# Optimization experiments

Measured on AMD Instinct MI355X. Metric: run time of the kernel, lower is better.

Reference implementation:

```python
import jax, jax.numpy as jnp
import numpy as np

EMBED = 512
MLP_DIM = 2048
B, T = 4, 4096
EPS = 1e-5


def setup_inputs() -> dict:
    key = jax.random.key(0)
    ks = jax.random.split(key, 8)
    s = lambda fan_in: 1.0 / np.sqrt(fan_in)
    inp = {
        "x": jax.random.normal(ks[0], (B, T, EMBED), dtype=jnp.float32),
        "Wq": jax.random.uniform(ks[1], (EMBED, EMBED), jnp.float32, -s(EMBED), s(EMBED)),
        "bq": jnp.zeros((EMBED,), jnp.float32),
        "Wk": jax.random.uniform(ks[2], (EMBED, EMBED), jnp.float32, -s(EMBED), s(EMBED)),
        "bk": jnp.zeros((EMBED,), jnp.float32),
        "Wv": jax.random.uniform(ks[3], (EMBED, EMBED), jnp.float32, -s(EMBED), s(EMBED)),
        "bv": jnp.zeros((EMBED,), jnp.float32),
        "W1": jax.random.uniform(ks[4], (EMBED, MLP_DIM), jnp.float32, -s(EMBED), s(EMBED)),
        "b1": jnp.zeros((MLP_DIM,), jnp.float32),
        "W2": jax.random.uniform(ks[5], (MLP_DIM, EMBED), jnp.float32, -s(MLP_DIM), s(MLP_DIM)),
        "b2": jnp.zeros((EMBED,), jnp.float32),
        "ln1_g": jnp.ones((EMBED,), jnp.float32),
        "ln1_b": jnp.zeros((EMBED,), jnp.float32),
        "ln2_g": jnp.ones((EMBED,), jnp.float32),
        "ln2_b": jnp.zeros((EMBED,), jnp.float32),
    }
    return inp


def _layernorm(x, g, b):
    mu = x.mean(-1, keepdims=True)
    var = ((x - mu) ** 2).mean(-1, keepdims=True)
    return (x - mu) * jax.lax.rsqrt(var + EPS) * g + b


def reference(x, Wq, bq, Wk, bk, Wv, bv, W1, b1, W2, b2, ln1_g, ln1_b, ln2_g, ln2_b):
    # pre-LN causal self-attention (single head)
    h = _layernorm(x, ln1_g, ln1_b)
    q = h @ Wq + bq  # [B,T,D]
    k = h @ Wk + bk
    v = h @ Wv + bv
    scale = 1.0 / jnp.sqrt(jnp.float32(EMBED))
    scores = jnp.einsum("btd,bsd->bts", q, k) * scale  # [B,T,T]
    mask = jnp.tril(jnp.ones((T, T), dtype=bool))
    scores = jnp.where(mask, scores, -jnp.inf)
    # NOTE: source applies softmax over the ENTIRE [T,T] matrix per batch
    # element (global max + global sum), not per-row. Replicate exactly.
    m = scores.max(axis=(-2, -1), keepdims=True)
    e = jnp.exp(scores - m)
    attn = e / e.sum(axis=(-2, -1), keepdims=True)
    x = x + jnp.einsum("bts,bsd->btd", attn, v)
    # MLP
    h2 = _layernorm(x, ln2_g, ln2_b)
    x = x + (jax.nn.gelu(h2 @ W1 + b1, approximate=False) @ W2 + b2)
    return x
```

## Files before the change

kernel.cpp:

```cpp
#include <hip/hip_runtime.h>
#include <hip/hip_bf16.h>
#include <math.h>

#define EMBED 512
#define MLPD  2048
#define NB    4
#define TS    4096
#define BT    (NB*TS)
#define BK    64
#define NTILES_TRI 528

typedef __attribute__((ext_vector_type(4))) float f32x4;
typedef __attribute__((ext_vector_type(8))) short s16x8;
typedef __hip_bfloat16 bf16_t;

__device__ __forceinline__ void gload16(const void* g, void* l) {
  __builtin_amdgcn_global_load_lds(
      (const __attribute__((address_space(1))) void*)g,
      (__attribute__((address_space(3))) void*)l, 16, 0, 0);
}

__device__ __forceinline__ float fast_erf(float y) {
  const float ay = fabsf(y);
  const float t = __builtin_amdgcn_rcpf(1.0f + 0.3275911f*ay);
  float poly = 1.061405429f;
  poly = poly*t - 1.453152027f;
  poly = poly*t + 1.421413741f;
  poly = poly*t - 0.284496736f;
  poly = poly*t + 0.254829592f;
  poly = poly*t;
  const float e = 1.0f - poly*__expf(-ay*ay);
  return copysignf(e, y);
}


__device__ __forceinline__ void gemm_core(
    const bf16_t* __restrict__ A, int lda,
    const bf16_t* __restrict__ Bt, int ldb,
    int kmax, bf16_t* Alds, bf16_t* Blds, f32x4 acc[4][4])
{
  const int tid = threadIdx.x;
  const int w  = tid >> 6;
  const int l  = tid & 63;
  const int wr = w >> 1, wc = w & 1;
  const int fr = l & 15, fg = l >> 4;

  #pragma unroll
  for (int i = 0; i < 4; ++i)
    #pragma unroll
    for (int j = 0; j < 4; ++j)
      #pragma unroll
      for (int e = 0; e < 4; ++e)
        acc[i][j][e] = 0.0f;

  const int srow = w*32 + (l >> 3);
  const int sx = (((l & 7) ^ ((l >> 3) & 7)))*8;
  const int rsw = fr & 7;

  for (int k0 = 0; k0 < kmax; k0 += BK) {
    __syncthreads();
    #pragma unroll
    for (int c = 0; c < 4; ++c) {
      const bf16_t* ga = A  + (size_t)(srow + c*8)*lda + (k0 + sx);
      const bf16_t* gb = Bt + (size_t)(srow + c*8)*ldb + (k0 + sx);
      gload16(ga, Alds + (w*32 + c*8)*BK);
      gload16(gb, Blds + (w*32 + c*8)*BK);
    }
    __syncthreads();
    #pragma unroll
    for (int kk = 0; kk < BK; kk += 32) {
      s16x8 av[4], bv[4];
      const int ch = (kk >> 3) + fg;
      const int co = (ch ^ rsw) << 3;
      #pragma unroll
      for (int mf = 0; mf < 4; ++mf)
        av[mf] = *(const s16x8*)(Alds + (wr*64 + mf*16 + fr)*BK + co);
      #pragma unroll
      for (int nf = 0; nf < 4; ++nf)
        bv[nf] = *(const s16x8*)(Blds + (wc*64 + nf*16 + fr)*BK + co);
      #pragma unroll
      for (int mf = 0; mf < 4; ++mf)
        #pragma unroll
        for (int nf = 0; nf < 4; ++nf)
          acc[mf][nf] = __builtin_amdgcn_mfma_f32_16x16x32_bf16(
              av[mf], bv[nf], acc[mf][nf], 0, 0, 0);
    }
  }
}

__device__ __forceinline__ void gemm_core_deep(
    const bf16_t* __restrict__ A, int lda,
    const bf16_t* __restrict__ Bt, int ldb,
    int kmax, bf16_t* Alds, bf16_t* Blds, f32x4 acc[4][4])
{
  const int tid = threadIdx.x;
  const int w  = tid >> 6;
  const int l  = tid & 63;
  const int wr = w >> 1, wc = w & 1;
  const int fr = l & 15, fg = l >> 4;

  #pragma unroll
  for (int i = 0; i < 4; ++i)
    #pragma unroll
    for (int j = 0; j < 4; ++j)
      #pragma unroll
      for (int e = 0; e < 4; ++e)
        acc[i][j][e] = 0.0f;

  const int srow = w*32 + (l >> 3);
  const int sx = (((l & 7) ^ ((l >> 3) & 7)))*8;
  const int rsw = fr & 7;
  const int T = kmax >> 6;

  #define ISSUE_A(t_) do { \
    bf16_t* dst = Alds + ((t_) % 3)*(128*BK); \
    const int k0_ = (t_)*BK; \
    _Pragma("unroll") \
    for (int c = 0; c < 4; ++c) \
      gload16(A + (size_t)(srow + c*8)*lda + (k0_ + sx), dst + (w*32 + c*8)*BK); \
  } while (0)
  #define ISSUE_B(t_) do { \
    bf16_t* dst = Blds + ((t_) & 1)*(128*BK); \
    const int k0_ = (t_)*BK; \
    _Pragma("unroll") \
    for (int c = 0; c < 4; ++c) \
      gload16(Bt + (size_t)(srow + c*8)*ldb + (k0_ + sx), dst + (w*32 + c*8)*BK); \
  } while (0)

  ISSUE_A(0); ISSUE_B(0);
  if (T > 1) ISSUE_A(1);

  for (int t = 0; t < T; ++t) {
    if (t <= T - 3) {
      ISSUE_B(t + 1); ISSUE_A(t + 2);
      asm volatile("s_waitcnt vmcnt(12)" ::: "memory");
    } else if (t == T - 2) {
      ISSUE_B(t + 1);
      asm volatile("s_waitcnt vmcnt(8)" ::: "memory");
    } else {
      asm volatile("s_waitcnt vmcnt(0)" ::: "memory");
    }
    __builtin_amdgcn_s_barrier();
    bf16_t* Ac = Alds + (t % 3)*(128*BK);
    bf16_t* Bc = Blds + (t & 1)*(128*BK);
    #pragma unroll
    for (int kk = 0; kk < BK; kk += 32) {
      s16x8 av[4], bv[4];
      const int ch = (kk >> 3) + fg;
      const int co = (ch ^ rsw) << 3;
      #pragma unroll
      for (int mf = 0; mf < 4; ++mf)
        av[mf] = *(const s16x8*)(Ac + (wr*64 + mf*16 + fr)*BK + co);
      #pragma unroll
      for (int nf = 0; nf < 4; ++nf)
        bv[nf] = *(const s16x8*)(Bc + (wc*64 + nf*16 + fr)*BK + co);
      #pragma unroll
      for (int mf = 0; mf < 4; ++mf)
        #pragma unroll
        for (int nf = 0; nf < 4; ++nf)
          acc[mf][nf] = __builtin_amdgcn_mfma_f32_16x16x32_bf16(
              av[mf], bv[nf], acc[mf][nf], 0, 0, 0);
    }
    __builtin_amdgcn_s_barrier();
  }
  #undef ISSUE_A
  #undef ISSUE_B
}

#define EPILOGUE_SETUP \
  const int l = threadIdx.x & 63; const int w = threadIdx.x >> 6; \
  const int wr = w >> 1, wc = w & 1, fr = l & 15, fg = l >> 4;

__global__ void __launch_bounds__(256) k_proj_qkv(
    const bf16_t* __restrict__ A,
    const bf16_t* __restrict__ wqt, const bf16_t* __restrict__ wkt,
    const bf16_t* __restrict__ wvt,
    const float* __restrict__ bq, const float* __restrict__ bk,
    const float* __restrict__ bv,
    bf16_t* __restrict__ qb, bf16_t* __restrict__ kb, bf16_t* __restrict__ vt)
{
  __shared__ __align__(16) bf16_t Alds[128*BK];
  __shared__ __align__(16) bf16_t Blds[128*BK];
  f32x4 acc[4][4];
  const int z = blockIdx.z;
  const bf16_t* Wt = (z == 0) ? wqt : (z == 1) ? wkt : wvt;
  const float* bias = (z == 0) ? bq : (z == 1) ? bk : bv;
  const int m0 = blockIdx.x*128, n0 = blockIdx.y*128;
  gemm_core(A + (size_t)m0*EMBED, EMBED, Wt + (size_t)n0*EMBED, EMBED, EMBED,
            Alds, Blds, acc);
  EPILOGUE_SETUP
  if (z < 2) {
    bf16_t* outp = (z == 0) ? qb : kb;
    #pragma unroll
    for (int mf = 0; mf < 4; ++mf)
      #pragma unroll
      for (int nf = 0; nf < 4; ++nf) {
        const int col = n0 + wc*64 + nf*16 + fr;
        const float bb = bias[col];
        #pragma unroll
        for (int j = 0; j < 4; ++j) {
          const int row = m0 + wr*64 + mf*16 + fg*4 + j;
          outp[(size_t)row*EMBED + col] = __float2bfloat16(acc[mf][nf][j] + bb);
        }
      }
  } else {
    #pragma unroll
    for (int mf = 0; mf < 4; ++mf)
      #pragma unroll
      for (int nf = 0; nf < 4; ++nf) {
        const int col = n0 + wc*64 + nf*16 + fr;
        const float bb = bias[col];
        #pragma unroll
        for (int j = 0; j < 4; ++j) {
          const int row = m0 + wr*64 + mf*16 + fg*4 + j;
          const int b = row >> 12, t = row & 4095;
          vt[((size_t)b*EMBED + col)*TS + t] = __float2bfloat16(acc[mf][nf][j] + bb);
        }
      }
  }
}

__global__ void __launch_bounds__(256) k_attn1(
    const bf16_t* __restrict__ q, const bf16_t* __restrict__ kmat,
    bf16_t* __restrict__ P, float* __restrict__ partials, int serial_b)
{
  __shared__ __align__(16) bf16_t Alds[128*BK];
  __shared__ __align__(16) bf16_t Blds[128*BK];
  int b, r;
  if (serial_b >= 0) {
    b = serial_b; r = blockIdx.x;
  } else {
    const int L = blockIdx.x;
    const int logical = (L & 7)*264 + (L >> 3);
    b = logical / NTILES_TRI;
    r = logical - b*NTILES_TRI;
  }
  int ti = (int)((sqrtf(8.0f*(float)r + 1.0f) - 1.0f)*0.5f);
  while ((ti + 1)*(ti + 2)/2 <= r) ++ti;
  while (ti*(ti + 1)/2 > r) --ti;
  const int tj = r - ti*(ti + 1)/2;

  f32x4 acc[4][4];
  const bf16_t* A  = q    + ((size_t)b*TS + (size_t)ti*128)*EMBED;
  const bf16_t* Bt = kmat + ((size_t)b*TS + (size_t)tj*128)*EMBED;
  gemm_core(A, EMBED, Bt, EMBED, EMBED, Alds, Blds, acc);

  EPILOGUE_SETUP
  bf16_t* Pb = P + (size_t)((serial_b >= 0) ? 0 : b)*TS*TS;
  const float SC = 0.044194173824159216f;
  float lsum = 0.0f;
  #pragma unroll
  for (int mf = 0; mf < 4; ++mf)
    #pragma unroll
    for (int nf = 0; nf < 4; ++nf) {
      const int gs = tj*128 + wc*64 + nf*16 + fr;
      #pragma unroll
      for (int j = 0; j < 4; ++j) {
        const int gt = ti*128 + wr*64 + mf*16 + fg*4 + j;
        float e = 0.0f;
        if (gs <= gt) e = __expf(acc[mf][nf][j]*SC - 30.0f);
        Pb[(size_t)gt*TS + gs] = __float2bfloat16(e);
        lsum += e;
      }
    }
  #pragma unroll
  for (int off = 32; off > 0; off >>= 1) lsum += __shfl_xor(lsum, off);
  __shared__ float red[4];
  if (l == 0) red[w] = lsum;
  __syncthreads();
  if (threadIdx.x == 0)
    partials[(size_t)b*NTILES_TRI + r] = red[0] + red[1] + red[2] + red[3];
}

__global__ void k_reduce(const float* __restrict__ part, float* __restrict__ S, int n)
{
  const int b = blockIdx.x;
  const int l = threadIdx.x;
  float s = 0.0f;
  for (int i = l; i < n; i += 64) s += part[(size_t)b*n + i];
  #pragma unroll
  for (int off = 32; off > 0; off >>= 1) s += __shfl_xor(s, off);
  if (l == 0) S[b] = s;
}

__global__ void __launch_bounds__(256) k_attn2(
    const bf16_t* __restrict__ P, const bf16_t* __restrict__ vt,
    const float* __restrict__ S, const float* __restrict__ x,
    float* __restrict__ out, int serial_b)
{
  __shared__ __align__(16) bf16_t Alds[3*128*BK];
  __shared__ __align__(16) bf16_t Blds[2*128*BK];
  int ti, nj, b;
  if (serial_b >= 0) {
    ti = blockIdx.x; nj = blockIdx.y; b = serial_b;
  } else {
    const int L = blockIdx.x;
    const int xc = L & 7;
    const int idx = L >> 3;
    nj = idx & 3;
    const int s = idx >> 2;
    b = s & 3;
    const int which = s >> 2;
    ti = (which == 0) ? 2*xc
       : (which == 1) ? 2*xc + 1
       : (which == 2) ? 30 - 2*xc
                      : 31 - 2*xc;
  }
  f32x4 acc[4][4];
  const bf16_t* A  = P + (size_t)((serial_b >= 0) ? 0 : b)*TS*TS + (size_t)ti*128*TS;
  const bf16_t* Bt = vt + ((size_t)b*EMBED + (size_t)nj*128)*TS;
  const int kmax = (ti + 1)*128;
  gemm_core_deep(A, TS, Bt, TS, kmax, Alds, Blds, acc);

  EPILOGUE_SETUP
  const float invS = 1.0f / S[b];
  #pragma unroll
  for (int mf = 0; mf < 4; ++mf)
    #pragma unroll
    for (int nf = 0; nf < 4; ++nf) {
      const int d = nj*128 + wc*64 + nf*16 + fr;
      #pragma unroll
      for (int j = 0; j < 4; ++j) {
        const int t = ti*128 + wr*64 + mf*16 + fg*4 + j;
        const size_t idx2 = ((size_t)b*TS + t)*EMBED + d;
        out[idx2] = x[idx2] + acc[mf][nf][j]*invS;
      }
    }
}

__global__ void __launch_bounds__(256) k_mlp1(
    const bf16_t* __restrict__ A, const bf16_t* __restrict__ Wt,
    const float* __restrict__ bias, bf16_t* __restrict__ mid)
{
  __shared__ __align__(16) bf16_t Alds[128*BK];
  __shared__ __align__(16) bf16_t Blds[128*BK];
  f32x4 acc[4][4];
  const int m0 = blockIdx.x*128, n0 = blockIdx.y*128;
  gemm_core(A + (size_t)m0*EMBED, EMBED, Wt + (size_t)n0*EMBED, EMBED, EMBED,
            Alds, Blds, acc);
  EPILOGUE_SETUP
  #pragma unroll
  for (int mf = 0; mf < 4; ++mf)
    #pragma unroll
    for (int nf = 0; nf < 4; ++nf) {
      const int col = n0 + wc*64 + nf*16 + fr;
      const float bb = bias[col];
      #pragma unroll
      for (int j = 0; j < 4; ++j) {
        const int row = m0 + wr*64 + mf*16 + fg*4 + j;
        const float pre = acc[mf][nf][j] + bb;
        const float ge = 0.5f*pre*(1.0f + fast_erf(pre*0.70710678118654752f));
        mid[(size_t)row*MLPD + col] = __float2bfloat16(ge);
      }
    }
}

__global__ void __launch_bounds__(256) k_mlp2(
    const bf16_t* __restrict__ A, const bf16_t* __restrict__ Wt,
    const float* __restrict__ bias, float* __restrict__ out)
{
  __shared__ __align__(16) bf16_t Alds[3*128*BK];
  __shared__ __align__(16) bf16_t Blds[2*128*BK];
  f32x4 acc[4][4];
  const int m0 = blockIdx.x*128, n0 = blockIdx.y*128;
  gemm_core_deep(A + (size_t)m0*MLPD, MLPD, Wt + (size_t)n0*MLPD, MLPD, MLPD,
                 Alds, Blds, acc);
  EPILOGUE_SETUP
  #pragma unroll
  for (int mf = 0; mf < 4; ++mf)
    #pragma unroll
    for (int nf = 0; nf < 4; ++nf) {
      const int col = n0 + wc*64 + nf*16 + fr;
      const float bb = bias[col];
      #pragma unroll
      for (int j = 0; j < 4; ++j) {
        const int row = m0 + wr*64 + mf*16 + fg*4 + j;
        const size_t idx = (size_t)row*EMBED + col;
        out[idx] = out[idx] + acc[mf][nf][j] + bb;
      }
    }
}

__global__ void __launch_bounds__(256) k_ln(
    const float* __restrict__ x, const float* __restrict__ g,
    const float* __restrict__ bta, bf16_t* __restrict__ h)
{
  const int row = blockIdx.x*4 + (threadIdx.x >> 6);
  const int l = threadIdx.x & 63;
  const float4* xr = (const float4*)(x + (size_t)row*EMBED);
  const float4 a = xr[l*2], c = xr[l*2 + 1];
  float vals[8] = {a.x, a.y, a.z, a.w, c.x, c.y, c.z, c.w};
  float s = 0.0f, ss = 0.0f;
  #pragma unroll
  for (int i = 0; i < 8; ++i) { s += vals[i]; ss += vals[i]*vals[i]; }
  #pragma unroll
  for (int off = 32; off > 0; off >>= 1) {
    s  += __shfl_xor(s,  off);
    ss += __shfl_xor(ss, off);
  }
  const float mu = s*(1.0f/EMBED);
  const float var = ss*(1.0f/EMBED) - mu*mu;
  const float rs = rsqrtf(var + 1e-5f);
  const float4* g4 = (const float4*)g;
  const float4* b4 = (const float4*)bta;
  const float4 ga = g4[l*2], gc = g4[l*2 + 1];
  const float4 ba = b4[l*2], bc = b4[l*2 + 1];
  const float gv[8] = {ga.x, ga.y, ga.z, ga.w, gc.x, gc.y, gc.z, gc.w};
  const float bv[8] = {ba.x, ba.y, ba.z, ba.w, bc.x, bc.y, bc.z, bc.w};
  s16x8 ov;
  bf16_t* ovp = (bf16_t*)&ov;
  #pragma unroll
  for (int i = 0; i < 8; ++i)
    ovp[i] = __float2bfloat16((vals[i] - mu)*rs*gv[i] + bv[i]);
  *((s16x8*)(h + (size_t)row*EMBED) + l) = ov;
}

__global__ void __launch_bounds__(256) k_transpose_all(
    const float* __restrict__ Wq, const float* __restrict__ Wk,
    const float* __restrict__ Wv, const float* __restrict__ W1,
    const float* __restrict__ W2,
    bf16_t* __restrict__ wqt, bf16_t* __restrict__ wkt,
    bf16_t* __restrict__ wvt, bf16_t* __restrict__ w1t,
    bf16_t* __restrict__ w2t)
{
  __shared__ float tile[32][33];
  int L = blockIdx.x;
  const float* W; bf16_t* Wt; int Kd, Nd, t;
  if (L < 768) {
    const int m = L >> 8; t = L & 255;
    W  = (m == 0) ? Wq : (m == 1) ? Wk : Wv;
    Wt = (m == 0) ? wqt : (m == 1) ? wkt : wvt;
    Kd = EMBED; Nd = EMBED;
  } else if (L < 1792) {
    t = L - 768;  W = W1; Wt = w1t; Kd = EMBED; Nd = MLPD;
  } else {
    t = L - 1792; W = W2; Wt = w2t; Kd = MLPD; Nd = EMBED;
  }
  const int ntx = Nd >> 5;
  const int tx32 = (t % ntx)*32, ty32 = (t / ntx)*32;
  const int x = threadIdx.x & 31, y8 = threadIdx.x >> 5;
  #pragma unroll
  for (int r = 0; r < 4; ++r) {
    const int y = y8 + r*8;
    tile[y][x] = W[(size_t)(ty32 + y)*Nd + tx32 + x];
  }
  __syncthreads();
  #pragma unroll
  for (int r = 0; r < 4; ++r) {
    const int y = y8 + r*8;
    Wt[(size_t)(tx32 + y)*Kd + ty32 + x] = __float2bfloat16(tile[x][y]);
  }
}

extern "C" void kernel_launch(void* const* d_in, const int* in_sizes, int n_in,
                              void* d_out, int out_size, void* d_ws, size_t ws_size,
                              hipStream_t stream) {
  (void)in_sizes; (void)n_in; (void)out_size;
  const float* x   = (const float*)d_in[0];
  const float* Wq  = (const float*)d_in[1];
  const float* bq  = (const float*)d_in[2];
  const float* Wk  = (const float*)d_in[3];
  const float* bk  = (const float*)d_in[4];
  const float* Wv  = (const float*)d_in[5];
  const float* bv  = (const float*)d_in[6];
  const float* W1  = (const float*)d_in[7];
  const float* b1  = (const float*)d_in[8];
  const float* W2  = (const float*)d_in[9];
  const float* b2  = (const float*)d_in[10];
  const float* g1  = (const float*)d_in[11];
  const float* be1 = (const float*)d_in[12];
  const float* g2  = (const float*)d_in[13];
  const float* be2 = (const float*)d_in[14];
  float* out = (float*)d_out;

  char* p = (char*)d_ws;
  auto alloc = [&](size_t bytes) -> char* {
    char* r = p; p += (bytes + 255) & ~(size_t)255; return r;
  };
  bf16_t* h   = (bf16_t*)alloc((size_t)BT*EMBED*2);
  bf16_t* wqt = (bf16_t*)alloc((size_t)EMBED*EMBED*2);
  bf16_t* wkt = (bf16_t*)alloc((size_t)EMBED*EMBED*2);
  bf16_t* wvt = (bf16_t*)alloc((size_t)EMBED*EMBED*2);
  bf16_t* w1t = (bf16_t*)alloc((size_t)MLPD*EMBED*2);
  bf16_t* w2t = (bf16_t*)alloc((size_t)EMBED*MLPD*2);
  bf16_t* qb  = (bf16_t*)alloc((size_t)BT*EMBED*2);
  bf16_t* kb  = (bf16_t*)alloc((size_t)BT*EMBED*2);
  bf16_t* vtb = (bf16_t*)alloc((size_t)BT*EMBED*2);
  float* partials = (float*)alloc((size_t)NB*NTILES_TRI*sizeof(float));
  float* S = (float*)alloc(256);

  const size_t mid_bytes = (size_t)BT*MLPD*2;
  const size_t p_full    = (size_t)NB*TS*TS*2;
  const size_t used = (size_t)(p - (char*)d_ws);
  const bool full = ws_size >= used + (p_full > mid_bytes ? p_full : mid_bytes);
  char* region = alloc(full ? p_full : mid_bytes);
  bf16_t* P   = (bf16_t*)region;
  bf16_t* mid = (bf16_t*)region;

  k_transpose_all<<<dim3(2816), 256, 0, stream>>>(Wq, Wk, Wv, W1, W2,
                                                  wqt, wkt, wvt, w1t, w2t);
  k_ln<<<BT/4, 256, 0, stream>>>(x, g1, be1, h);

  k_proj_qkv<<<dim3(BT/128, EMBED/128, 3), 256, 0, stream>>>(
      h, wqt, wkt, wvt, bq, bk, bv, qb, kb, vtb);

  if (full) {
    k_attn1<<<dim3(NB*NTILES_TRI), 256, 0, stream>>>(qb, kb, P, partials, -1);
    k_reduce<<<NB, 64, 0, stream>>>(partials, S, NTILES_TRI);
    k_attn2<<<dim3(512), 256, 0, stream>>>(P, vtb, S, x, out, -1);
  } else {
    for (int b = 0; b < NB; ++b) {
      k_attn1<<<dim3(NTILES_TRI), 256, 0, stream>>>(qb, kb, P, partials, b);
      k_reduce<<<1, 64, 0, stream>>>(partials + (size_t)b*NTILES_TRI, S + b, NTILES_TRI);
      k_attn2<<<dim3(TS/128, EMBED/128), 256, 0, stream>>>(P, vtb, S, x, out, b);
    }
  }

  k_ln<<<BT/4, 256, 0, stream>>>(out, g2, be2, h);
  k_mlp1<<<dim3(BT/128, MLPD/128), 256, 0, stream>>>(h, w1t, b1, mid);
  k_mlp2<<<dim3(BT/128, EMBED/128), 256, 0, stream>>>(mid, w2t, b2, out);
}
```

Baseline: 297.0 us.

## Pair complementary causal row tiles per block in attention-V GEMM for load balance

Each attn2 block now processes two row tiles (ti and 31-ti), so every block does the same total K length over the causal triangle. The grid shrinks from 512 to 256 blocks, matching the MI355X CU count, so the imbalanced tail of the triangular workload goes away. In exchange each block runs two serial GEMMs, and with fewer blocks there is less latency hiding between waves. The mapping of nj and b is also reorganized.

```diff
diff --git a/kernel.cpp b/kernel.cpp
--- a/kernel.cpp
+++ b/kernel.cpp
@@ -290,42 +290,44 @@
 {
   __shared__ __align__(16) bf16_t Alds[3*128*BK];
   __shared__ __align__(16) bf16_t Blds[2*128*BK];
-  int ti, nj, b;
+  int nj, b, ti0, ti1, nt;
   if (serial_b >= 0) {
-    ti = blockIdx.x; nj = blockIdx.y; b = serial_b;
+    ti0 = blockIdx.x; ti1 = 0; nj = blockIdx.y; b = serial_b; nt = 1;
   } else {
     const int L = blockIdx.x;
     const int xc = L & 7;
-    const int idx = L >> 3;
-    nj = idx & 3;
-    const int s = idx >> 2;
-    b = s & 3;
-    const int which = s >> 2;
-    ti = (which == 0) ? 2*xc
-       : (which == 1) ? 2*xc + 1
-       : (which == 2) ? 30 - 2*xc
-                      : 31 - 2*xc;
-  }
-  f32x4 acc[4][4];
-  const bf16_t* A  = P + (size_t)((serial_b >= 0) ? 0 : b)*TS*TS + (size_t)ti*128*TS;
+    const int i  = L >> 3;
+    const int combo = i >> 4;
+    const int pp = i & 15;
+    const int njb = xc*2 + combo;
+    nj = njb & 3; b = njb >> 2;
+    ti0 = 31 - pp;
+    ti1 = pp;
+    nt = 2;
+  }
+  const size_t pbase = (size_t)((serial_b >= 0) ? 0 : b)*TS*TS;
   const bf16_t* Bt = vt + ((size_t)b*EMBED + (size_t)nj*128)*TS;
-  const int kmax = (ti + 1)*128;
-  gemm_core_deep(A, TS, Bt, TS, kmax, Alds, Blds, acc);
-
+  const float invS = 1.0f / S[b];
   EPILOGUE_SETUP
-  const float invS = 1.0f / S[b];
-  #pragma unroll
-  for (int mf = 0; mf < 4; ++mf)
-    #pragma unroll
-    for (int nf = 0; nf < 4; ++nf) {
-      const int d = nj*128 + wc*64 + nf*16 + fr;
-      #pragma unroll
-      for (int j = 0; j < 4; ++j) {
-        const int t = ti*128 + wr*64 + mf*16 + fg*4 + j;
-        const size_t idx2 = ((size_t)b*TS + t)*EMBED + d;
-        out[idx2] = x[idx2] + acc[mf][nf][j]*invS;
+
+  for (int q = 0; q < nt; ++q) {
+    const int ti = (q == 0) ? ti0 : ti1;
+    f32x4 acc[4][4];
+    const bf16_t* A = P + pbase + (size_t)ti*128*TS;
+    gemm_core_deep(A, TS, Bt, TS, (ti + 1)*128, Alds, Blds, acc);
+    #pragma unroll
+    for (int mf = 0; mf < 4; ++mf)
+      #pragma unroll
+      for (int nf = 0; nf < 4; ++nf) {
+        const int d = nj*128 + wc*64 + nf*16 + fr;
+        #pragma unroll
+        for (int j = 0; j < 4; ++j) {
+          const int t = ti*128 + wr*64 + mf*16 + fg*4 + j;
+          const size_t idx2 = ((size_t)b*TS + t)*EMBED + d;
+          out[idx2] = x[idx2] + acc[mf][nf][j]*invS;
+        }
       }
-    }
+  }
 }
 
 __global__ void __launch_bounds__(256) k_mlp1(
@@ -507,7 +509,7 @@
   if (full) {
     k_attn1<<<dim3(NB*NTILES_TRI), 256, 0, stream>>>(qb, kb, P, partials, -1);
     k_reduce<<<NB, 64, 0, stream>>>(partials, S, NTILES_TRI);
-    k_attn2<<<dim3(512), 256, 0, stream>>>(P, vtb, S, x, out, -1);
+    k_attn2<<<dim3(256), 256, 0, stream>>>(P, vtb, S, x, out, -1);
   } else {
     for (int b = 0; b < NB; ++b) {
       k_attn1<<<dim3(NTILES_TRI), 256, 0, stream>>>(qb, kb, P, partials, b);
```

Measured after the change: 298.7 us. Within noise of the previous version (+0.6%).

## Stage attention P tile through swizzled LDS and remap GEMM blocks per XCD

Applied to the files above, without the earlier changes.

The attention score kernel now writes its exp tile into a swizzled LDS buffer, reusing the GEMM staging space, and then stores it to global memory as coalesced 16-byte rows. This replaces scattered 2-byte strided stores to the large P matrix. The QKV, MLP1 and MLP2 GEMMs also remap block indices so that consecutive row tiles land on the same XCD, and MLP1 moves to a 1D grid, to improve L2 reuse of shared A/B tiles. The cost is extra LDS traffic and two more barriers in the attention epilogue.

```diff
diff --git a/kernel.cpp b/kernel.cpp
--- a/kernel.cpp
+++ b/kernel.cpp
@@ -185,7 +185,9 @@
   const int z = blockIdx.z;
   const bf16_t* Wt = (z == 0) ? wqt : (z == 1) ? wkt : wvt;
   const float* bias = (z == 0) ? bq : (z == 1) ? bk : bv;
-  const int m0 = blockIdx.x*128, n0 = blockIdx.y*128;
+  const int bx = blockIdx.x;
+  const int m0 = ((bx & 7)*16 + (bx >> 3))*128;
+  const int n0 = blockIdx.y*128;
   gemm_core(A + (size_t)m0*EMBED, EMBED, Wt + (size_t)n0*EMBED, EMBED, EMBED,
             Alds, Blds, acc);
   EPILOGUE_SETUP
@@ -224,8 +226,10 @@
     const bf16_t* __restrict__ q, const bf16_t* __restrict__ kmat,
     bf16_t* __restrict__ P, float* __restrict__ partials, int serial_b)
 {
-  __shared__ __align__(16) bf16_t Alds[128*BK];
-  __shared__ __align__(16) bf16_t Blds[128*BK];
+  __shared__ __align__(16) bf16_t LB[2][128*BK];
+  bf16_t* Alds = LB[0];
+  bf16_t* Blds = LB[1];
+  bf16_t* Plds = &LB[0][0];
   int b, r;
   if (serial_b >= 0) {
     b = serial_b; r = blockIdx.x;
@@ -246,23 +250,39 @@
   gemm_core(A, EMBED, Bt, EMBED, EMBED, Alds, Blds, acc);
 
   EPILOGUE_SETUP
-  bf16_t* Pb = P + (size_t)((serial_b >= 0) ? 0 : b)*TS*TS;
+  __syncthreads();
   const float SC = 0.044194173824159216f;
   float lsum = 0.0f;
   #pragma unroll
   for (int mf = 0; mf < 4; ++mf)
     #pragma unroll
     for (int nf = 0; nf < 4; ++nf) {
-      const int gs = tj*128 + wc*64 + nf*16 + fr;
+      const int ls = wc*64 + nf*16 + fr;
+      const int gs = tj*128 + ls;
+      const int chs = ((ls >> 3) ^ ((wr*64 + mf*16 + fg*4) & 7));
+      (void)chs;
       #pragma unroll
       for (int j = 0; j < 4; ++j) {
-        const int gt = ti*128 + wr*64 + mf*16 + fg*4 + j;
+        const int lt = wr*64 + mf*16 + fg*4 + j;
+        const int gt = ti*128 + lt;
         float e = 0.0f;
         if (gs <= gt) e = __expf(acc[mf][nf][j]*SC - 30.0f);
-        Pb[(size_t)gt*TS + gs] = __float2bfloat16(e);
+        const int sc = (((ls >> 3) ^ (lt & 7)) << 3) | (ls & 7);
+        Plds[lt*128 + sc] = __float2bfloat16(e);
         lsum += e;
       }
     }
+  __syncthreads();
+  bf16_t* Pb = P + (size_t)((serial_b >= 0) ? 0 : b)*TS*TS
+                 + (size_t)ti*128*TS + tj*128;
+  #pragma unroll
+  for (int it = 0; it < 8; ++it) {
+    const int row = w*32 + it*4 + (l >> 4);
+    const int ch  = l & 15;
+    const int chs2 = (ch & 8) | ((ch ^ (row & 7)) & 7);
+    const s16x8 v = *(const s16x8*)(Plds + row*128 + chs2*8);
+    *(s16x8*)(Pb + (size_t)row*TS + ch*8) = v;
+  }
   #pragma unroll
   for (int off = 32; off > 0; off >>= 1) lsum += __shfl_xor(lsum, off);
   __shared__ float red[4];
@@ -335,7 +355,11 @@
   __shared__ __align__(16) bf16_t Alds[128*BK];
   __shared__ __align__(16) bf16_t Blds[128*BK];
   f32x4 acc[4][4];
-  const int m0 = blockIdx.x*128, n0 = blockIdx.y*128;
+  const int L = blockIdx.x;
+  const int xc = L & 7;
+  const int i  = L >> 3;
+  const int m0 = (xc*16 + (i & 15))*128;
+  const int n0 = (i >> 4)*128;
   gemm_core(A + (size_t)m0*EMBED, EMBED, Wt + (size_t)n0*EMBED, EMBED, EMBED,
             Alds, Blds, acc);
   EPILOGUE_SETUP
@@ -362,7 +386,9 @@
   __shared__ __align__(16) bf16_t Alds[3*128*BK];
   __shared__ __align__(16) bf16_t Blds[2*128*BK];
   f32x4 acc[4][4];
-  const int m0 = blockIdx.x*128, n0 = blockIdx.y*128;
+  const int bx = blockIdx.x;
+  const int m0 = ((bx & 7)*16 + (bx >> 3))*128;
+  const int n0 = blockIdx.y*128;
   gemm_core_deep(A + (size_t)m0*MLPD, MLPD, Wt + (size_t)n0*MLPD, MLPD, MLPD,
                  Alds, Blds, acc);
   EPILOGUE_SETUP
@@ -517,6 +543,6 @@
   }
 
   k_ln<<<BT/4, 256, 0, stream>>>(out, g2, be2, h);
-  k_mlp1<<<dim3(BT/128, MLPD/128), 256, 0, stream>>>(h, w1t, b1, mid);
+  k_mlp1<<<dim3(2048), 256, 0, stream>>>(h, w1t, b1, mid);
   k_mlp2<<<dim3(BT/128, EMBED/128), 256, 0, stream>>>(mid, w2t, b2, out);
 }
```

New measurement: 301.1 us. Within noise of the previous version (+1.4%).
